# Kernel tuning notes

Hardware: AMD Instinct MI355X
Metric: run time of the kernel (lower is better)

## Reference

```python
import jax, jax.numpy as jnp
import numpy as np


def _shift(x, axis, d):
    # value at voxel p becomes x[p + d*e_axis], zero outside the grid
    n = x.shape[axis]
    zero = jnp.zeros_like(jax.lax.slice_in_dim(x, 0, 1, axis=axis))
    if d > 0:
        return jnp.concatenate([jax.lax.slice_in_dim(x, 1, n, axis=axis), zero], axis=axis)
    return jnp.concatenate([zero, jax.lax.slice_in_dim(x, 0, n - 1, axis=axis)], axis=axis)


def _forward(coords, instance_gt, S, num_scales):
    # InputLayer mode=4: average features of duplicate coords.
    # features = [instance+1, 1]; averaging duplicates of [v,1] gives [mean(v), 1].
    inst = instance_gt.astype(jnp.float32) + 1.0
    c = coords.astype(jnp.int32)
    flat = (c[:, 0] * S + c[:, 1]) * S + c[:, 2]
    ssum = jnp.zeros(S * S * S, jnp.float32).at[flat].add(inst)
    cnt = jnp.zeros(S * S * S, jnp.float32).at[flat].add(1.0)
    val = (ssum / jnp.maximum(cnt, 1.0)).reshape(S, S, S)   # mean label per active voxel, 0 if inactive
    act = (cnt > 0).astype(jnp.float32).reshape(S, S, S)    # active-site mask
    outs = []
    for scale in range(num_scales):
        if scale == 0:
            v, a = val, act
        else:
            f = 2 ** scale
            Ss = S // f
            # scn AveragePooling divides by pool volume; features[:, :1]/count then
            # renormalizes -> mean of val over ACTIVE fine voxels in the block.
            vsum = val.reshape(Ss, f, Ss, f, Ss, f).sum(axis=(1, 3, 5))
            asum = act.reshape(Ss, f, Ss, f, Ss, f).sum(axis=(1, 3, 5))
            a = (asum > 0).astype(jnp.float32)
            v = vsum / jnp.maximum(asum, 1.0)
        va = v * a
        feats = []
        masks = []
        # one-hot submanifold conv kernel offsets (4,22,10,16,12,14) = (-x,+x,-y,+y,-z,+z)
        for axis in range(3):
            for d in (-1, 1):
                sh = _shift(va, axis, d)                      # neighbor value, 0 if neighbor inactive
                feats.append((jnp.abs(sh - v) < 0.01).astype(jnp.float32))
                masks.append((sh > 0).astype(jnp.float32))
        # submanifold conv is only defined at active sites -> mask by a
        out = jnp.stack(feats + masks, axis=-1) * a[..., None]  # [Ss,Ss,Ss,12]
        outs.append(out.reshape(-1, 12))
    return jnp.concatenate(outs, axis=0)


def setup_inputs() -> dict:
    key = jax.random.key(0)
    k1, k2 = jax.random.split(key)
    N, S = 4_000_000, 128
    coords = jax.random.randint(k1, (N, 3), 0, S, dtype=jnp.int32)
    instance_gt = jax.random.randint(k2, (N,), 0, 50).astype(jnp.float32)
    return {"coords": coords, "instance_gt": instance_gt, "inputScale": S, "numScales": 6}


def reference(coords, instance_gt, inputScale, numScales):
    return _forward(coords, instance_gt, inputScale, numScales)
```

## Files before the change

kernel.cpp:

```cpp
#include <hip/hip_runtime.h>

#define GS3 2097152
#define NS1 262144
#define NS2 32768
#define NS3 4096
#define NS4 512
#define NS5 64
#define NSALL 299584

#define OB1 25165824
#define OB2 28311552
#define OB3 28704768
#define OB4 28753920
#define OB5 28760064

#define NREG 512
#define RVOX 4096
#define CAP  10240
#define PPB  8192
#define RPT  (PPB / 256)


__global__ __launch_bounds__(256) void zero_cnt_kernel(unsigned int* __restrict__ cnt) {
  cnt[threadIdx.x] = 0u;
  cnt[threadIdx.x + 256] = 0u;
}

__global__ __launch_bounds__(256) void bin_kernel(
    const int* __restrict__ coords, const float* __restrict__ inst,
    unsigned int* __restrict__ cnt, unsigned int* __restrict__ bins, int N) {
  __shared__ unsigned srec[PPB];
  __shared__ unsigned hist[NREG];
  __shared__ unsigned lofs[NREG];
  __shared__ unsigned basec[NREG];
  __shared__ unsigned part[256];
  __shared__ unsigned total_sh;
  unsigned vrec[RPT];
  int tid = threadIdx.x;
  int start = blockIdx.x * PPB;
  for (int j = tid; j < NREG; j += 256) hist[j] = 0;
  __syncthreads();
#pragma unroll
  for (int j = 0; j < RPT; j++) {
    int i = start + j * 256 + tid;
    unsigned v = 0xFFFFFFFFu;
    if (i < N) {
      int x = coords[3 * i + 0];
      int y = coords[3 * i + 1];
      int z = coords[3 * i + 2];
      unsigned lab = (unsigned)inst[i] + 1u;
      unsigned r = (((unsigned)x >> 1) << 3) | ((unsigned)y >> 4);
      unsigned l = (((unsigned)x & 1) << 11) | (((unsigned)y & 15) << 7) | (unsigned)z;
      v = (r << 18) | (l << 6) | lab;
      atomicAdd(&hist[r], 1u);
    }
    vrec[j] = v;
  }
  __syncthreads();
  unsigned ha = hist[2 * tid], hb = hist[2 * tid + 1];
  part[tid] = ha + hb;
  __syncthreads();
  for (int o = 1; o < 256; o <<= 1) {
    unsigned v = part[tid];
    unsigned add = (tid >= o) ? part[tid - o] : 0u;
    __syncthreads();
    part[tid] = v + add;
    __syncthreads();
  }
  unsigned inc = part[tid];
  unsigned ex = inc - (ha + hb);
  lofs[2 * tid] = ex;
  lofs[2 * tid + 1] = ex + ha;
  if (tid == 255) total_sh = inc;
  __syncthreads();
  for (int j = tid; j < NREG; j += 256) {
    unsigned h = hist[j];
    basec[j] = h ? atomicAdd(&cnt[j], h) : 0u;
  }
  __syncthreads();
  for (int j = tid; j < NREG; j += 256) hist[j] = 0;
  __syncthreads();
#pragma unroll
  for (int j = 0; j < RPT; j++) {
    unsigned v = vrec[j];
    if (v != 0xFFFFFFFFu) {
      unsigned r = v >> 18;
      unsigned pos = lofs[r] + atomicAdd(&hist[r], 1u);
      srec[pos] = v;
    }
  }
  __syncthreads();
  unsigned total = total_sh;
  for (unsigned j = tid; j < total; j += 256) {
    unsigned v = srec[j];
    unsigned r = v >> 18;
    unsigned p = basec[r] + (j - lofs[r]);
    if (p < CAP) bins[r * CAP + p] = v & 0x3FFFFu;
  }
}

__global__ __launch_bounds__(256) void build_pool_kernel(
    const unsigned int* __restrict__ cnt, const unsigned int* __restrict__ bins,
    unsigned int* __restrict__ P,
    double* __restrict__ vs1, double* __restrict__ as1) {
  __shared__ unsigned grid[RVOX];
  int r = blockIdx.x;
  int tid = threadIdx.x;
  for (int j = tid; j < RVOX; j += 256) grid[j] = 0;
  __syncthreads();
  int n = min((int)cnt[r], CAP);
  for (int k = tid; k < n; k += 256) {
    unsigned v = bins[r * CAP + k];
    atomicAdd(&grid[v >> 6], (1u << 20) | (v & 63u));
  }
  __syncthreads();
  int X = r >> 3, yo = r & 7;
  unsigned pbase = ((unsigned)(2 * X) << 14) | ((unsigned)yo << 11);
  for (int j = tid; j < RVOX; j += 256) {
    P[pbase + ((j >> 11) << 14) + (j & 0x7FF)] = grid[j];
  }
  for (int c = tid; c < 512; c += 256) {
    int yl = c >> 6, Z = c & 63;
    double vs = 0.0, as = 0.0;
#pragma unroll
    for (int dx = 0; dx < 2; dx++)
#pragma unroll
      for (int dy = 0; dy < 2; dy++)
#pragma unroll
        for (int dz = 0; dz < 2; dz++) {
          int j = (dx << 11) | ((2 * yl + dy) << 7) | (2 * Z + dz);
          unsigned pk = grid[j];
          unsigned cc = pk >> 20;
          if (cc) {
            vs += (double)(pk & 0xFFFFFu) / (double)cc;
            as += 1.0;
          }
        }
    int q = (X << 12) | (((yo << 3) + yl) << 6) | Z;
    vs1[q] = vs;
    as1[q] = as;
  }
}

__global__ __launch_bounds__(256) void poolRest_kernel(
    const double* __restrict__ vs1, const double* __restrict__ as1,
    double* __restrict__ vs2, double* __restrict__ as2,
    double* __restrict__ vs3, double* __restrict__ as3,
    double* __restrict__ vs4, double* __restrict__ as4,
    double* __restrict__ vs5, double* __restrict__ as5) {
  int t = blockIdx.x * blockDim.x + threadIdx.x;

  if (t < NS2) {
    int q = t;
    int X = q >> 10, Y = (q >> 5) & 31, Z = q & 31;
    double vs = 0.0, as = 0.0;
#pragma unroll
    for (int dx = 0; dx < 2; dx++)
#pragma unroll
      for (int dy = 0; dy < 2; dy++)
#pragma unroll
        for (int dz = 0; dz < 2; dz++) {
          int p = ((((X << 1) + dx) << 12) + (((Y << 1) + dy) << 6) + ((Z << 1) + dz));
          vs += vs1[p];
          as += as1[p];
        }
    vs2[q] = vs;
    as2[q] = as;
    return;
  }
  t -= NS2;
  if (t < NS3) {
    int q = t;
    int X = q >> 8, Y = (q >> 4) & 15, Z = q & 15;
    double vs = 0.0, as = 0.0;
    for (int dx = 0; dx < 4; dx++)
      for (int dy = 0; dy < 4; dy++)
#pragma unroll
        for (int dz = 0; dz < 4; dz++) {
          int p = ((((X << 2) + dx) << 12) + (((Y << 2) + dy) << 6) + ((Z << 2) + dz));
          vs += vs1[p];
          as += as1[p];
        }
    vs3[q] = vs;
    as3[q] = as;
    return;
  }
  t -= NS3;
  if (t < NS4 * 64) {
    int w = t >> 6, lane = t & 63;
    int X = w >> 6, Y = (w >> 3) & 7, Z = w & 7;
    double vs = 0.0, as = 0.0;
#pragma unroll
    for (int j = 0; j < 8; j++) {
      int c = lane * 8 + j;
      int dx = c >> 6, dy = (c >> 3) & 7, dz = c & 7;
      int p = ((((X << 3) + dx) << 12) + (((Y << 3) + dy) << 6) + ((Z << 3) + dz));
      vs += vs1[p];
      as += as1[p];
    }
    for (int o = 32; o > 0; o >>= 1) {
      vs += __shfl_down(vs, o, 64);
      as += __shfl_down(as, o, 64);
    }
    if (lane == 0) { vs4[w] = vs; as4[w] = as; }
    return;
  }
  t -= NS4 * 64;
  if (t < NS5 * 64) {
    int w = t >> 6, lane = t & 63;
    int X = w >> 4, Y = (w >> 2) & 3, Z = w & 3;
    double vs = 0.0, as = 0.0;
    for (int j = 0; j < 64; j++) {
      int c = lane * 64 + j;
      int dx = c >> 8, dy = (c >> 4) & 15, dz = c & 15;
      int p = ((((X << 4) + dx) << 12) + (((Y << 4) + dy) << 6) + ((Z << 4) + dz));
      vs += vs1[p];
      as += as1[p];
    }
    for (int o = 32; o > 0; o >>= 1) {
      vs += __shfl_down(vs, o, 64);
      as += __shfl_down(as, o, 64);
    }
    if (lane == 0) { vs5[w] = vs; as5[w] = as; }
  }
}

__global__ __launch_bounds__(256) void out_kernel(
    const unsigned int* __restrict__ P,
    const double* __restrict__ vs1, const double* __restrict__ as1,
    const double* __restrict__ vs2, const double* __restrict__ as2,
    const double* __restrict__ vs3, const double* __restrict__ as3,
    const double* __restrict__ vs4, const double* __restrict__ as4,
    const double* __restrict__ vs5, const double* __restrict__ as5,
    float* __restrict__ out) {
  int p = blockIdx.x * blockDim.x + threadIdx.x;
  if (p < GS3) {
    unsigned pk = P[p];
    int cc = (int)(pk >> 20);
    float4 r0 = {0.f, 0.f, 0.f, 0.f}, r1 = r0, r2 = r0;
    if (cc) {
      int sc = (int)(pk & 0xFFFFFu);
      int x = p >> 14, y = (p >> 7) & 127, z = p & 127;
      const int off[6] = {-(1 << 14), (1 << 14), -(1 << 7), (1 << 7), -1, 1};
      const bool inb[6] = {x > 0, x < 127, y > 0, y < 127, z > 0, z < 127};
      float f[6], m[6];
#pragma unroll
      for (int k = 0; k < 6; k++) {
        int sn = 0, cn = 0;
        if (inb[k]) {
          unsigned pn = P[p + off[k]];
          cn = (int)(pn >> 20);
          sn = (int)(pn & 0xFFFFFu);
        }
        if (cn) {
          long long d = (long long)sn * cc - (long long)sc * cn;
          if (d < 0) d = -d;
          f[k] = (100ll * d < (long long)cn * cc) ? 1.f : 0.f;
          m[k] = 1.f;
        } else {
          f[k] = 0.f;
          m[k] = 0.f;
        }
      }
      r0 = {f[0], f[1], f[2], f[3]};
      r1 = {f[4], f[5], m[0], m[1]};
      r2 = {m[2], m[3], m[4], m[5]};
    }
    float4* o = (float4*)(out + 12ll * p);
    o[0] = r0; o[1] = r1; o[2] = r2;
    return;
  }
  int t = p - GS3;
  const double *vs, *as;
  int ls, q;
  long long obase;
  if (t < NS1) { q = t; vs = vs1; as = as1; ls = 6; obase = OB1; }
  else if (t < NS1 + NS2) { q = t - NS1; vs = vs2; as = as2; ls = 5; obase = OB2; }
  else if (t < NS1 + NS2 + NS3) { q = t - NS1 - NS2; vs = vs3; as = as3; ls = 4; obase = OB3; }
  else if (t < NS1 + NS2 + NS3 + NS4) { q = t - NS1 - NS2 - NS3; vs = vs4; as = as4; ls = 3; obase = OB4; }
  else if (t < NSALL) { q = t - NS1 - NS2 - NS3 - NS4; vs = vs5; as = as5; ls = 2; obase = OB5; }
  else return;

  int Ss = 1 << ls;
  int X = q >> (2 * ls), Y = (q >> ls) & (Ss - 1), Z = q & (Ss - 1);
  double ac = as[q];
  float4 r0 = {0.f, 0.f, 0.f, 0.f}, r1 = r0, r2 = r0;
  if (ac > 0.0) {
    double vc = vs[q] / ac;
    const int off[6] = {-(Ss * Ss), Ss * Ss, -Ss, Ss, -1, 1};
    const bool inb[6] = {X > 0, X < Ss - 1, Y > 0, Y < Ss - 1, Z > 0, Z < Ss - 1};
    float f[6], m[6];
#pragma unroll
    for (int k = 0; k < 6; k++) {
      double van = 0.0;
      if (inb[k]) {
        double an = as[q + off[k]];
        if (an > 0.0) van = vs[q + off[k]] / an;
      }
      f[k] = (fabs(van - vc) < 0.01) ? 1.f : 0.f;
      m[k] = (van > 0.0) ? 1.f : 0.f;
    }
    r0 = {f[0], f[1], f[2], f[3]};
    r1 = {f[4], f[5], m[0], m[1]};
    r2 = {m[2], m[3], m[4], m[5]};
  }
  float4* o = (float4*)(out + obase + 12ll * q);
  o[0] = r0; o[1] = r1; o[2] = r2;
}

extern "C" void kernel_launch(void* const* d_in, const int* in_sizes, int n_in,
                              void* d_out, int out_size, void* d_ws, size_t ws_size,
                              hipStream_t stream) {
  const int* coords = (const int*)d_in[0];
  const float* inst = (const float*)d_in[1];
  int N = in_sizes[1];
  float* out = (float*)d_out;

  char* base = (char*)d_ws;
  unsigned int* P = (unsigned int*)base;
  double* vs1 = (double*)(base + 8388608);
  double* as1 = vs1 + NS1;
  double* vs2 = as1 + NS1; double* as2 = vs2 + NS2;
  double* vs3 = as2 + NS2; double* as3 = vs3 + NS3;
  double* vs4 = as3 + NS3; double* as4 = vs4 + NS4;
  double* vs5 = as4 + NS4; double* as5 = vs5 + NS5;
  size_t cnt_off = 13182976;
  unsigned int* cnt  = (unsigned int*)(base + cnt_off);
  unsigned int* bins = (unsigned int*)(base + cnt_off + 2048);
  size_t need = cnt_off + 2048 + (size_t)NREG * CAP * 4;
  if (ws_size < need) return;

  int nchunks = (N + PPB - 1) / PPB;
  zero_cnt_kernel<<<1, 256, 0, stream>>>(cnt);
  bin_kernel<<<nchunks, 256, 0, stream>>>(coords, inst, cnt, bins, N);
  build_pool_kernel<<<NREG, 256, 0, stream>>>(cnt, bins, P, vs1, as1);
  poolRest_kernel<<<(NS2 + NS3 + NS4 * 64 + NS5 * 64 + 255) / 256, 256, 0, stream>>>(
      vs1, as1, vs2, as2, vs3, as3, vs4, as4, vs5, as5);
  out_kernel<<<(GS3 + NSALL + 255) / 256, 256, 0, stream>>>(
      P, vs1, as1, vs2, as2, vs3, as3, vs4, as4, vs5, as5, out);
}
```

Measured before the change: 99.90 us.

## Replace global atomic bin counters with per-chunk fixed-capacity bin slots

Each binning block now writes its per-region points into its own fixed slot of 64 entries per region and records the clamped count. This removes the global atomicAdd counters and the separate zeroing kernel launch. The pooling kernel then walks every chunk's slot for its region, one chunk per thread, serially. The trade-offs are less coalesced, load-imbalanced reads in the pooling step, a much larger workspace, and silent point loss if a region gets more than 64 points in one chunk.

```diff
diff --git a/kernel.cpp b/kernel.cpp
--- a/kernel.cpp
+++ b/kernel.cpp
@@ -16,28 +16,23 @@
 
 #define NREG 512
 #define RVOX 4096
-#define CAP  10240
 #define PPB  8192
 #define RPT  (PPB / 256)
-
-
-__global__ __launch_bounds__(256) void zero_cnt_kernel(unsigned int* __restrict__ cnt) {
-  cnt[threadIdx.x] = 0u;
-  cnt[threadIdx.x + 256] = 0u;
-}
+#define CAPB 64
+
 
 __global__ __launch_bounds__(256) void bin_kernel(
     const int* __restrict__ coords, const float* __restrict__ inst,
-    unsigned int* __restrict__ cnt, unsigned int* __restrict__ bins, int N) {
+    unsigned int* __restrict__ counts, unsigned int* __restrict__ bins, int N) {
   __shared__ unsigned srec[PPB];
   __shared__ unsigned hist[NREG];
   __shared__ unsigned lofs[NREG];
-  __shared__ unsigned basec[NREG];
   __shared__ unsigned part[256];
   __shared__ unsigned total_sh;
   unsigned vrec[RPT];
   int tid = threadIdx.x;
-  int start = blockIdx.x * PPB;
+  int bid = blockIdx.x;
+  int start = bid * PPB;
   for (int j = tid; j < NREG; j += 256) hist[j] = 0;
   __syncthreads();
 #pragma unroll
@@ -58,6 +53,8 @@
   }
   __syncthreads();
   unsigned ha = hist[2 * tid], hb = hist[2 * tid + 1];
+  counts[(size_t)bid * NREG + 2 * tid]     = ha < CAPB ? ha : CAPB;
+  counts[(size_t)bid * NREG + 2 * tid + 1] = hb < CAPB ? hb : CAPB;
   part[tid] = ha + hb;
   __syncthreads();
   for (int o = 1; o < 256; o <<= 1) {
@@ -73,11 +70,6 @@
   lofs[2 * tid + 1] = ex + ha;
   if (tid == 255) total_sh = inc;
   __syncthreads();
-  for (int j = tid; j < NREG; j += 256) {
-    unsigned h = hist[j];
-    basec[j] = h ? atomicAdd(&cnt[j], h) : 0u;
-  }
-  __syncthreads();
   for (int j = tid; j < NREG; j += 256) hist[j] = 0;
   __syncthreads();
 #pragma unroll
@@ -91,27 +83,31 @@
   }
   __syncthreads();
   unsigned total = total_sh;
+  size_t bbase = (size_t)bid * NREG * CAPB;
   for (unsigned j = tid; j < total; j += 256) {
     unsigned v = srec[j];
     unsigned r = v >> 18;
-    unsigned p = basec[r] + (j - lofs[r]);
-    if (p < CAP) bins[r * CAP + p] = v & 0x3FFFFu;
+    unsigned p = j - lofs[r];
+    if (p < CAPB) bins[bbase + r * CAPB + p] = v & 0x3FFFFu;
   }
 }
 
 __global__ __launch_bounds__(256) void build_pool_kernel(
-    const unsigned int* __restrict__ cnt, const unsigned int* __restrict__ bins,
+    const unsigned int* __restrict__ counts, const unsigned int* __restrict__ bins,
     unsigned int* __restrict__ P,
-    double* __restrict__ vs1, double* __restrict__ as1) {
+    double* __restrict__ vs1, double* __restrict__ as1, int nchunks) {
   __shared__ unsigned grid[RVOX];
   int r = blockIdx.x;
   int tid = threadIdx.x;
   for (int j = tid; j < RVOX; j += 256) grid[j] = 0;
   __syncthreads();
-  int n = min((int)cnt[r], CAP);
-  for (int k = tid; k < n; k += 256) {
-    unsigned v = bins[r * CAP + k];
-    atomicAdd(&grid[v >> 6], (1u << 20) | (v & 63u));
+  for (int b = tid; b < nchunks; b += 256) {
+    int cb = (int)counts[(size_t)b * NREG + r];
+    const unsigned* src = bins + ((size_t)b * NREG + r) * CAPB;
+    for (int k = 0; k < cb; k++) {
+      unsigned v = src[k];
+      atomicAdd(&grid[v >> 6], (1u << 20) | (v & 63u));
+    }
   }
   __syncthreads();
   int X = r >> 3, yo = r & 7;
@@ -315,6 +311,7 @@
   const float* inst = (const float*)d_in[1];
   int N = in_sizes[1];
   float* out = (float*)d_out;
+  int nchunks = (N + PPB - 1) / PPB;
 
   char* base = (char*)d_ws;
   unsigned int* P = (unsigned int*)base;
@@ -324,16 +321,15 @@
   double* vs3 = as2 + NS2; double* as3 = vs3 + NS3;
   double* vs4 = as3 + NS3; double* as4 = vs4 + NS4;
   double* vs5 = as4 + NS4; double* as5 = vs5 + NS5;
-  size_t cnt_off = 13182976;
-  unsigned int* cnt  = (unsigned int*)(base + cnt_off);
-  unsigned int* bins = (unsigned int*)(base + cnt_off + 2048);
-  size_t need = cnt_off + 2048 + (size_t)NREG * CAP * 4;
+  size_t counts_off = 13182976;
+  unsigned int* counts = (unsigned int*)(base + counts_off);
+  size_t bins_off = counts_off + ((size_t)nchunks * NREG * 4 + 1023) / 1024 * 1024;
+  unsigned int* bins = (unsigned int*)(base + bins_off);
+  size_t need = bins_off + (size_t)nchunks * NREG * CAPB * 4;
   if (ws_size < need) return;
 
-  int nchunks = (N + PPB - 1) / PPB;
-  zero_cnt_kernel<<<1, 256, 0, stream>>>(cnt);
-  bin_kernel<<<nchunks, 256, 0, stream>>>(coords, inst, cnt, bins, N);
-  build_pool_kernel<<<NREG, 256, 0, stream>>>(cnt, bins, P, vs1, as1);
+  bin_kernel<<<nchunks, 256, 0, stream>>>(coords, inst, counts, bins, N);
+  build_pool_kernel<<<NREG, 256, 0, stream>>>(counts, bins, P, vs1, as1, nchunks);
   poolRest_kernel<<<(NS2 + NS3 + NS4 * 64 + NS5 * 64 + 255) / 256, 256, 0, stream>>>(
       vs1, as1, vs2, as2, vs3, as3, vs4, as4, vs5, as5);
   out_kernel<<<(GS3 + NSALL + 255) / 256, 256, 0, stream>>>(
```

After: 86.41 us, median of 2. 1.16x faster.
